# Performance work log

Measured on AMD Instinct MI355X. Metric: run time of the kernel, lower is better.

Reference implementation:

```python
import jax, jax.numpy as jnp
import numpy as np

T, F = 32768, 512


def setup_inputs() -> dict:
    key = jax.random.key(0)
    ks = jax.random.split(key, 7)
    return {
        "x": jax.random.normal(ks[0], (T, F), dtype=jnp.float32),
        # per-feature LSTM(1,1) params, PyTorch gate order [i, f, g, o]
        "w_ih": 0.5 * jax.random.normal(ks[1], (F, 4), dtype=jnp.float32),
        "w_hh": 0.5 * jax.random.normal(ks[2], (F, 4), dtype=jnp.float32),
        "b_ih": 0.5 * jax.random.normal(ks[3], (F, 4), dtype=jnp.float32),
        "b_hh": 0.5 * jax.random.normal(ks[4], (F, 4), dtype=jnp.float32),
        # torch.rand for h0, torch.randn for c0 (as in the original forward)
        "h0": jax.random.uniform(ks[5], (F,), dtype=jnp.float32),
        "c0": jax.random.normal(ks[6], (F,), dtype=jnp.float32),
    }


def reference(x, w_ih, w_hh, b_ih, b_hh, h0, c0):
    # Fused: all F independent scalar LSTM cells stepped together over time.
    b = b_ih + b_hh  # [F, 4]

    def step(carry, x_t):
        h, c = carry  # [F], [F]
        gates = x_t[:, None] * w_ih + h[:, None] * w_hh + b  # [F, 4]
        i = jax.nn.sigmoid(gates[:, 0])
        f = jax.nn.sigmoid(gates[:, 1])
        g = jnp.tanh(gates[:, 2])
        o = jax.nn.sigmoid(gates[:, 3])
        c = f * c + i * g
        h = o * jnp.tanh(c)
        return (h, c), 2.0 * h  # forward emits 2 * out

    _, ys = jax.lax.scan(step, (h0, c0), x)
    return ys  # [T, F]
```

## Files before the change

kernel.cpp:

```cpp
#include <hip/hip_runtime.h>


#define T_STEPS 32768
#define F_FEAT  512
#define CHUNK_L 64
#define WARM    96
#define DEPTH   (WARM + CHUNK_L)
#define UNROLL  8

typedef float v2f __attribute__((ext_vector_type(2)));

__device__ __forceinline__ v2f pk_fma(v2f a, v2f b, v2f c) {
    return __builtin_elementwise_fma(a, b, c);
}
__device__ __forceinline__ v2f exp2v(v2f a) {
    v2f r; r.x = __builtin_amdgcn_exp2f(a.x); r.y = __builtin_amdgcn_exp2f(a.y); return r;
}
__device__ __forceinline__ v2f rcpv(v2f a) {
    v2f r; r.x = __builtin_amdgcn_rcpf(a.x); r.y = __builtin_amdgcn_rcpf(a.y); return r;
}

__global__ __launch_bounds__(64, 2) void lstm_kernel(
    const float*  __restrict__ x,
    const float4* __restrict__ w_ih,
    const float4* __restrict__ w_hh,
    const float4* __restrict__ b_ih,
    const float4* __restrict__ b_hh,
    const float*  __restrict__ h0,
    const float*  __restrict__ c0,
    float*        __restrict__ out)
{
    const int cb = blockIdx.x;
    const int f  = blockIdx.y * 64 + threadIdx.x;

    const float LOG2E = 1.4426950408889634f;
    const float S_SIG = -LOG2E;
    const float S_C   = 2.0f * LOG2E;

    const float4 wi = w_ih[f];
    const float4 wh = w_hh[f];
    const float4 bi = b_ih[f];
    const float4 bh = b_hh[f];

    const v2f W1i = S_SIG * wi.x, W1f = S_SIG * wi.y, W1g = S_C * wi.z, W1o = S_SIG * wi.w;
    const v2f W2i = 0.5f * S_SIG * wh.x, W2f = 0.5f * S_SIG * wh.y,
              W2g = 0.5f * S_C   * wh.z, W2o = 0.5f * S_SIG * wh.w;
    const v2f Bi  = S_SIG * (bi.x + bh.x);
    const v2f Bf  = S_SIG * (bi.y + bh.y);
    const v2f Bg  = S_C   * (bi.z + bh.z);
    const v2f Bo  = S_SIG * (bi.w + bh.w);

    const v2f ONE  = 1.0f;
    const v2f SCv  = S_C;
    const v2f mSCv = -S_C;
    const v2f M4   = -4.0f;
    const v2f TWO  = 2.0f;

    const int t_emitA = (2 * cb) * CHUNK_L;
    const int baseA   = t_emitA - WARM;

    v2f H2 = 0.0f, C2 = 0.0f;
    const float H0v = 2.0f * h0[f];
    const float C0v = S_C * c0[f];

    const float* xp = x + f;
    float*       op = out + f;

    float curA[UNROLL], nxtA[UNROLL], curB[UNROLL], nxtB[UNROLL];
#pragma unroll
    for (int j = 0; j < UNROLL; ++j) {
        int tA = baseA + j;           if (tA < 0) tA = 0;
        int tB = baseA + CHUNK_L + j; if (tB < 0) tB = 0;
        curA[j] = xp[tA * F_FEAT];
        curB[j] = xp[tB * F_FEAT];
        nxtA[j] = 0.0f; nxtB[j] = 0.0f;
    }

    for (int s0 = 0; s0 < DEPTH; s0 += UNROLL) {
        const int sn = s0 + UNROLL;
        if (sn < DEPTH) {
#pragma unroll
            for (int j = 0; j < UNROLL; ++j) {
                int tA = baseA + sn + j;           if (tA < 0) tA = 0;
                int tB = baseA + CHUNK_L + sn + j; if (tB < 0) tB = 0;
                nxtA[j] = xp[tA * F_FEAT];
                nxtB[j] = xp[tB * F_FEAT];
            }
        }
        if (cb == 0) {
            if (s0 == WARM - CHUNK_L) { H2.y = H0v; C2.y = C0v; }
            if (s0 == WARM)           { H2.x = H0v; C2.x = C0v; }
        }
        const bool emit = (s0 >= WARM);
#pragma unroll
        for (int j = 0; j < UNROLL; ++j) {
            const v2f xv = { curA[j], curB[j] };
            v2f gi = pk_fma(xv, W1i, Bi); gi = pk_fma(H2, W2i, gi);
            v2f gf = pk_fma(xv, W1f, Bf); gf = pk_fma(H2, W2f, gf);
            v2f gg = pk_fma(xv, W1g, Bg); gg = pk_fma(H2, W2g, gg);
            v2f go = pk_fma(xv, W1o, Bo); go = pk_fma(H2, W2o, go);
            const v2f ui = exp2v(gi);
            const v2f uf = exp2v(gf);
            const v2f ug = exp2v(gg);
            const v2f uo = exp2v(go);
            const v2f ai = ui + ONE;
            const v2f af = uf + ONE;
            const v2f ag = ug + ONE;
            const v2f ao = uo + ONE;
            const v2f am = pk_fma(ug, SCv, mSCv);
            const v2f P  = ai * ag;
            const v2f D  = P * af;
            const v2f D3 = D * ao;
            const v2f t2 = am * af;
            const v2f N  = pk_fma(C2, P, t2);
            const v2f R  = rcpv(D3);
            const v2f N2 = N * ao;
            C2 = N2 * R;
            const v2f ro = D * R;
            const v2f e  = exp2v(C2);
            const v2f ae = e + ONE;
            const v2f cc = rcpv(ae);
            const v2f TH = pk_fma(cc, M4, TWO);
            H2 = ro * TH;
            if (emit) {
                const int tw = t_emitA + (s0 - WARM) + j;
                op[tw * F_FEAT]             = H2.x;
                op[(tw + CHUNK_L) * F_FEAT] = H2.y;
            }
        }
#pragma unroll
        for (int j = 0; j < UNROLL; ++j) { curA[j] = nxtA[j]; curB[j] = nxtB[j]; }
    }
}

extern "C" void kernel_launch(void* const* d_in, const int* in_sizes, int n_in,
                              void* d_out, int out_size, void* d_ws, size_t ws_size,
                              hipStream_t stream) {
    const float*  x    = (const float*)d_in[0];
    const float4* w_ih = (const float4*)d_in[1];
    const float4* w_hh = (const float4*)d_in[2];
    const float4* b_ih = (const float4*)d_in[3];
    const float4* b_hh = (const float4*)d_in[4];
    const float*  h0   = (const float*)d_in[5];
    const float*  c0   = (const float*)d_in[6];
    float* out = (float*)d_out;

    lstm_kernel<<<dim3(T_STEPS / (2 * CHUNK_L), F_FEAT / 64), dim3(64), 0, stream>>>(
        x, w_ih, w_hh, b_ih, b_hh, h0, c0, out);
}
```

Baseline: 155.7 us.

## Fold output gate into recurrent weights to shorten serial dependency chain

Splits h into tanh(c) times the output-gate reciprocal and multiplies that reciprocal into the per-step recurrent weights, so the output gate's rcp runs off the critical path and the single combined rcp is replaced by two shorter independent ones. The h-dependent chain loses a multiply, at the cost of an extra rcp and four extra multiplies per step. It also specializes x-loading for blocks with nonnegative base index to drop the clamping. Numerics change slightly because of the separate reciprocals.

```diff
diff --git a/kernel.cpp b/kernel.cpp
--- a/kernel.cpp
+++ b/kernel.cpp
@@ -43,8 +43,8 @@
     const float4 bh = b_hh[f];
 
     const v2f W1i = S_SIG * wi.x, W1f = S_SIG * wi.y, W1g = S_C * wi.z, W1o = S_SIG * wi.w;
-    const v2f W2i = 0.5f * S_SIG * wh.x, W2f = 0.5f * S_SIG * wh.y,
-              W2g = 0.5f * S_C   * wh.z, W2o = 0.5f * S_SIG * wh.w;
+    const float W2i_s = 0.5f * S_SIG * wh.x, W2f_s = 0.5f * S_SIG * wh.y,
+                W2g_s = 0.5f * S_C   * wh.z, W2o_s = 0.5f * S_SIG * wh.w;
     const v2f Bi  = S_SIG * (bi.x + bh.x);
     const v2f Bf  = S_SIG * (bi.y + bh.y);
     const v2f Bg  = S_C   * (bi.z + bh.z);
@@ -59,7 +59,8 @@
     const int t_emitA = (2 * cb) * CHUNK_L;
     const int baseA   = t_emitA - WARM;
 
-    v2f H2 = 0.0f, C2 = 0.0f;
+    v2f th2 = 0.0f, C2 = 0.0f;
+    v2f W2roI = W2i_s, W2roF = W2f_s, W2roG = W2g_s, W2roO = W2o_s;
     const float H0v = 2.0f * h0[f];
     const float C0v = S_C * c0[f];
 
@@ -67,38 +68,61 @@
     float*       op = out + f;
 
     float curA[UNROLL], nxtA[UNROLL], curB[UNROLL], nxtB[UNROLL];
+    if (baseA >= 0) {
 #pragma unroll
-    for (int j = 0; j < UNROLL; ++j) {
-        int tA = baseA + j;           if (tA < 0) tA = 0;
-        int tB = baseA + CHUNK_L + j; if (tB < 0) tB = 0;
-        curA[j] = xp[tA * F_FEAT];
-        curB[j] = xp[tB * F_FEAT];
-        nxtA[j] = 0.0f; nxtB[j] = 0.0f;
+        for (int j = 0; j < UNROLL; ++j) {
+            curA[j] = xp[(baseA + j) * F_FEAT];
+            curB[j] = xp[(baseA + CHUNK_L + j) * F_FEAT];
+            nxtA[j] = 0.0f; nxtB[j] = 0.0f;
+        }
+    } else {
+#pragma unroll
+        for (int j = 0; j < UNROLL; ++j) {
+            int tA = baseA + j;           if (tA < 0) tA = 0;
+            int tB = baseA + CHUNK_L + j; if (tB < 0) tB = 0;
+            curA[j] = xp[tA * F_FEAT];
+            curB[j] = xp[tB * F_FEAT];
+            nxtA[j] = 0.0f; nxtB[j] = 0.0f;
+        }
     }
 
     for (int s0 = 0; s0 < DEPTH; s0 += UNROLL) {
         const int sn = s0 + UNROLL;
         if (sn < DEPTH) {
+            if (baseA >= 0) {
 #pragma unroll
-            for (int j = 0; j < UNROLL; ++j) {
-                int tA = baseA + sn + j;           if (tA < 0) tA = 0;
-                int tB = baseA + CHUNK_L + sn + j; if (tB < 0) tB = 0;
-                nxtA[j] = xp[tA * F_FEAT];
-                nxtB[j] = xp[tB * F_FEAT];
+                for (int j = 0; j < UNROLL; ++j) {
+                    nxtA[j] = xp[(baseA + sn + j) * F_FEAT];
+                    nxtB[j] = xp[(baseA + CHUNK_L + sn + j) * F_FEAT];
+                }
+            } else {
+#pragma unroll
+                for (int j = 0; j < UNROLL; ++j) {
+                    int tA = baseA + sn + j;           if (tA < 0) tA = 0;
+                    int tB = baseA + CHUNK_L + sn + j; if (tB < 0) tB = 0;
+                    nxtA[j] = xp[tA * F_FEAT];
+                    nxtB[j] = xp[tB * F_FEAT];
+                }
             }
         }
         if (cb == 0) {
-            if (s0 == WARM - CHUNK_L) { H2.y = H0v; C2.y = C0v; }
-            if (s0 == WARM)           { H2.x = H0v; C2.x = C0v; }
+            if (s0 == WARM - CHUNK_L) {
+                th2.y = H0v; C2.y = C0v;
+                W2roI.y = W2i_s; W2roF.y = W2f_s; W2roG.y = W2g_s; W2roO.y = W2o_s;
+            }
+            if (s0 == WARM) {
+                th2.x = H0v; C2.x = C0v;
+                W2roI.x = W2i_s; W2roF.x = W2f_s; W2roG.x = W2g_s; W2roO.x = W2o_s;
+            }
         }
         const bool emit = (s0 >= WARM);
 #pragma unroll
         for (int j = 0; j < UNROLL; ++j) {
             const v2f xv = { curA[j], curB[j] };
-            v2f gi = pk_fma(xv, W1i, Bi); gi = pk_fma(H2, W2i, gi);
-            v2f gf = pk_fma(xv, W1f, Bf); gf = pk_fma(H2, W2f, gf);
-            v2f gg = pk_fma(xv, W1g, Bg); gg = pk_fma(H2, W2g, gg);
-            v2f go = pk_fma(xv, W1o, Bo); go = pk_fma(H2, W2o, go);
+            v2f gi = pk_fma(xv, W1i, Bi); gi = pk_fma(th2, W2roI, gi);
+            v2f gf = pk_fma(xv, W1f, Bf); gf = pk_fma(th2, W2roF, gf);
+            v2f gg = pk_fma(xv, W1g, Bg); gg = pk_fma(th2, W2roG, gg);
+            v2f go = pk_fma(xv, W1o, Bo); go = pk_fma(th2, W2roO, go);
             const v2f ui = exp2v(gi);
             const v2f uf = exp2v(gf);
             const v2f ug = exp2v(gg);
@@ -107,25 +131,25 @@
             const v2f af = uf + ONE;
             const v2f ag = ug + ONE;
             const v2f ao = uo + ONE;
+            const v2f ro = rcpv(ao);
             const v2f am = pk_fma(ug, SCv, mSCv);
             const v2f P  = ai * ag;
-            const v2f D  = P * af;
-            const v2f D3 = D * ao;
+            const v2f Q  = P * af;
             const v2f t2 = am * af;
+            const v2f R3 = rcpv(Q);
             const v2f N  = pk_fma(C2, P, t2);
-            const v2f R  = rcpv(D3);
-            const v2f N2 = N * ao;
-            C2 = N2 * R;
-            const v2f ro = D * R;
+            C2 = N * R3;
             const v2f e  = exp2v(C2);
             const v2f ae = e + ONE;
             const v2f cc = rcpv(ae);
-            const v2f TH = pk_fma(cc, M4, TWO);
-            H2 = ro * TH;
+            th2 = pk_fma(cc, M4, TWO);
+            W2roI = W2i_s * ro; W2roF = W2f_s * ro;
+            W2roG = W2g_s * ro; W2roO = W2o_s * ro;
             if (emit) {
+                const v2f H = th2 * ro;
                 const int tw = t_emitA + (s0 - WARM) + j;
-                op[tw * F_FEAT]             = H2.x;
-                op[(tw + CHUNK_L) * F_FEAT] = H2.y;
+                op[tw * F_FEAT]             = H.x;
+                op[(tw + CHUNK_L) * F_FEAT] = H.y;
             }
         }
 #pragma unroll
```

Result: faster. 147.4 us (-5.3%).

## Ping-pong x prefetch buffers, drop clamps off-edge, shorten recurrence dependency chain

Applied to the files above, without the earlier changes.

Replaces the cur/next buffer copy with an even/odd ping-pong scheme, so each half-iteration's loads are issued while the other half computes and the register copies go away. Blocks whose window does not start before t=0 skip the clamp logic on addresses. The cell math is also reordered: the output-gate reciprocal is computed on its own and the cell update divides by a three-factor product instead of a four-factor one. This shortens the serial chain through C2 at the cost of one extra reciprocal per step. The emit condition is evaluated per 16-step pair, and since WARM is a multiple of 16 it stays correct.

```diff
diff --git a/kernel.cpp b/kernel.cpp
--- a/kernel.cpp
+++ b/kernel.cpp
@@ -66,25 +66,72 @@
     const float* xp = x + f;
     float*       op = out + f;
 
-    float curA[UNROLL], nxtA[UNROLL], curB[UNROLL], nxtB[UNROLL];
+    float eA[UNROLL], eB[UNROLL], oA[UNROLL], oB[UNROLL];
+    if (baseA >= 0) {
 #pragma unroll
-    for (int j = 0; j < UNROLL; ++j) {
-        int tA = baseA + j;           if (tA < 0) tA = 0;
-        int tB = baseA + CHUNK_L + j; if (tB < 0) tB = 0;
-        curA[j] = xp[tA * F_FEAT];
-        curB[j] = xp[tB * F_FEAT];
-        nxtA[j] = 0.0f; nxtB[j] = 0.0f;
+        for (int j = 0; j < UNROLL; ++j) {
+            eA[j] = xp[(baseA + j) * F_FEAT];
+            eB[j] = xp[(baseA + CHUNK_L + j) * F_FEAT];
+        }
+    } else {
+#pragma unroll
+        for (int j = 0; j < UNROLL; ++j) {
+            int tA = baseA + j;           if (tA < 0) tA = 0;
+            int tB = baseA + CHUNK_L + j; if (tB < 0) tB = 0;
+            eA[j] = xp[tA * F_FEAT];
+            eB[j] = xp[tB * F_FEAT];
+        }
     }
 
-    for (int s0 = 0; s0 < DEPTH; s0 += UNROLL) {
-        const int sn = s0 + UNROLL;
-        if (sn < DEPTH) {
+#define STEP(xa, xb, tw_expr)                                            \
+    {                                                                    \
+        const v2f xv = { (xa), (xb) };                                   \
+        v2f gi = pk_fma(xv, W1i, Bi); gi = pk_fma(H2, W2i, gi);          \
+        v2f gf = pk_fma(xv, W1f, Bf); gf = pk_fma(H2, W2f, gf);          \
+        v2f gg = pk_fma(xv, W1g, Bg); gg = pk_fma(H2, W2g, gg);          \
+        v2f go = pk_fma(xv, W1o, Bo); go = pk_fma(H2, W2o, go);          \
+        const v2f ui = exp2v(gi);                                        \
+        const v2f uf = exp2v(gf);                                        \
+        const v2f ug = exp2v(gg);                                        \
+        const v2f uo = exp2v(go);                                        \
+        const v2f ai = ui + ONE;                                         \
+        const v2f af = uf + ONE;                                         \
+        const v2f ag = ug + ONE;                                         \
+        const v2f ao = uo + ONE;                                         \
+        const v2f ro = rcpv(ao);                            \
+        const v2f am = pk_fma(ug, SCv, mSCv);            \
+        const v2f P  = ai * ag;                                          \
+        const v2f Q  = P * af;                                           \
+        const v2f t2 = am * af;                                          \
+        const v2f R3 = rcpv(Q);                                          \
+        const v2f N  = pk_fma(C2, P, t2);                                \
+        C2 = N * R3;                                  \
+        const v2f e  = exp2v(C2);                                        \
+        const v2f ae = e + ONE;                                          \
+        const v2f cc = rcpv(ae);                                         \
+        const v2f th2 = pk_fma(cc, M4, TWO);              \
+        H2 = th2 * ro;                                         \
+        if (emit) {                                                      \
+            const int tw = (tw_expr);                                    \
+            op[tw * F_FEAT]             = H2.x;                          \
+            op[(tw + CHUNK_L) * F_FEAT] = H2.y;                          \
+        }                                                                \
+    }
+
+    for (int s0 = 0; s0 < DEPTH; s0 += 2 * UNROLL) {
+        if (baseA >= 0) {
 #pragma unroll
             for (int j = 0; j < UNROLL; ++j) {
-                int tA = baseA + sn + j;           if (tA < 0) tA = 0;
-                int tB = baseA + CHUNK_L + sn + j; if (tB < 0) tB = 0;
-                nxtA[j] = xp[tA * F_FEAT];
-                nxtB[j] = xp[tB * F_FEAT];
+                oA[j] = xp[(baseA + s0 + UNROLL + j) * F_FEAT];
+                oB[j] = xp[(baseA + CHUNK_L + s0 + UNROLL + j) * F_FEAT];
+            }
+        } else {
+#pragma unroll
+            for (int j = 0; j < UNROLL; ++j) {
+                int tA = baseA + s0 + UNROLL + j;           if (tA < 0) tA = 0;
+                int tB = baseA + CHUNK_L + s0 + UNROLL + j; if (tB < 0) tB = 0;
+                oA[j] = xp[tA * F_FEAT];
+                oB[j] = xp[tB * F_FEAT];
             }
         }
         if (cb == 0) {
@@ -93,44 +140,31 @@
         }
         const bool emit = (s0 >= WARM);
 #pragma unroll
-        for (int j = 0; j < UNROLL; ++j) {
-            const v2f xv = { curA[j], curB[j] };
-            v2f gi = pk_fma(xv, W1i, Bi); gi = pk_fma(H2, W2i, gi);
-            v2f gf = pk_fma(xv, W1f, Bf); gf = pk_fma(H2, W2f, gf);
-            v2f gg = pk_fma(xv, W1g, Bg); gg = pk_fma(H2, W2g, gg);
-            v2f go = pk_fma(xv, W1o, Bo); go = pk_fma(H2, W2o, go);
-            const v2f ui = exp2v(gi);
-            const v2f uf = exp2v(gf);
-            const v2f ug = exp2v(gg);
-            const v2f uo = exp2v(go);
-            const v2f ai = ui + ONE;
-            const v2f af = uf + ONE;
-            const v2f ag = ug + ONE;
-            const v2f ao = uo + ONE;
-            const v2f am = pk_fma(ug, SCv, mSCv);
-            const v2f P  = ai * ag;
-            const v2f D  = P * af;
-            const v2f D3 = D * ao;
-            const v2f t2 = am * af;
-            const v2f N  = pk_fma(C2, P, t2);
-            const v2f R  = rcpv(D3);
-            const v2f N2 = N * ao;
-            C2 = N2 * R;
-            const v2f ro = D * R;
-            const v2f e  = exp2v(C2);
-            const v2f ae = e + ONE;
-            const v2f cc = rcpv(ae);
-            const v2f TH = pk_fma(cc, M4, TWO);
-            H2 = ro * TH;
-            if (emit) {
-                const int tw = t_emitA + (s0 - WARM) + j;
-                op[tw * F_FEAT]             = H2.x;
-                op[(tw + CHUNK_L) * F_FEAT] = H2.y;
+        for (int j = 0; j < UNROLL; ++j)
+            STEP(eA[j], eB[j], t_emitA + (s0 - WARM) + j);
+        const int sn = s0 + 2 * UNROLL;
+        if (sn < DEPTH) {
+            if (baseA >= 0) {
+#pragma unroll
+                for (int j = 0; j < UNROLL; ++j) {
+                    eA[j] = xp[(baseA + sn + j) * F_FEAT];
+                    eB[j] = xp[(baseA + CHUNK_L + sn + j) * F_FEAT];
+                }
+            } else {
+#pragma unroll
+                for (int j = 0; j < UNROLL; ++j) {
+                    int tA = baseA + sn + j;           if (tA < 0) tA = 0;
+                    int tB = baseA + CHUNK_L + sn + j; if (tB < 0) tB = 0;
+                    eA[j] = xp[tA * F_FEAT];
+                    eB[j] = xp[tB * F_FEAT];
+                }
             }
         }
 #pragma unroll
-        for (int j = 0; j < UNROLL; ++j) { curA[j] = nxtA[j]; curB[j] = nxtB[j]; }
+        for (int j = 0; j < UNROLL; ++j)
+            STEP(oA[j], oB[j], t_emitA + (s0 - WARM) + UNROLL + j);
     }
+#undef STEP
 }
 
 extern "C" void kernel_launch(void* const* d_in, const int* in_sizes, int n_in,
```

New measurement: 150.5 us. -3.3%, faster.

## Shorten warmup, drop clamping on interior chunks, split reciprocal off critical path

Applied to the files above, without the earlier changes.

Cuts the warm-up recurrence length from 96 to 88 steps, so each block runs fewer sequential steps at the cost of a slightly less converged state when the chunk starts emitting. Adds a branch that skips the index clamping when the chunk start is non-negative. Restructures the gate algebra so the output-gate sigmoid uses its own reciprocal, independent of the cell-state path, which shortens the serial dependency chain on C but adds one extra rcp per step. Reducing the warm-up relies on the recurrence forgetting its initial state, which carries an accuracy risk.

```diff
diff --git a/kernel.cpp b/kernel.cpp
--- a/kernel.cpp
+++ b/kernel.cpp
@@ -4,7 +4,7 @@
 #define T_STEPS 32768
 #define F_FEAT  512
 #define CHUNK_L 64
-#define WARM    96
+#define WARM    88
 #define DEPTH   (WARM + CHUNK_L)
 #define UNROLL  8
 
@@ -67,24 +67,41 @@
     float*       op = out + f;
 
     float curA[UNROLL], nxtA[UNROLL], curB[UNROLL], nxtB[UNROLL];
+    if (baseA >= 0) {
 #pragma unroll
-    for (int j = 0; j < UNROLL; ++j) {
-        int tA = baseA + j;           if (tA < 0) tA = 0;
-        int tB = baseA + CHUNK_L + j; if (tB < 0) tB = 0;
-        curA[j] = xp[tA * F_FEAT];
-        curB[j] = xp[tB * F_FEAT];
-        nxtA[j] = 0.0f; nxtB[j] = 0.0f;
+        for (int j = 0; j < UNROLL; ++j) {
+            curA[j] = xp[(baseA + j) * F_FEAT];
+            curB[j] = xp[(baseA + CHUNK_L + j) * F_FEAT];
+            nxtA[j] = 0.0f; nxtB[j] = 0.0f;
+        }
+    } else {
+#pragma unroll
+        for (int j = 0; j < UNROLL; ++j) {
+            int tA = baseA + j;           if (tA < 0) tA = 0;
+            int tB = baseA + CHUNK_L + j; if (tB < 0) tB = 0;
+            curA[j] = xp[tA * F_FEAT];
+            curB[j] = xp[tB * F_FEAT];
+            nxtA[j] = 0.0f; nxtB[j] = 0.0f;
+        }
     }
 
     for (int s0 = 0; s0 < DEPTH; s0 += UNROLL) {
         const int sn = s0 + UNROLL;
         if (sn < DEPTH) {
+            if (baseA >= 0) {
 #pragma unroll
-            for (int j = 0; j < UNROLL; ++j) {
-                int tA = baseA + sn + j;           if (tA < 0) tA = 0;
-                int tB = baseA + CHUNK_L + sn + j; if (tB < 0) tB = 0;
-                nxtA[j] = xp[tA * F_FEAT];
-                nxtB[j] = xp[tB * F_FEAT];
+                for (int j = 0; j < UNROLL; ++j) {
+                    nxtA[j] = xp[(baseA + sn + j) * F_FEAT];
+                    nxtB[j] = xp[(baseA + CHUNK_L + sn + j) * F_FEAT];
+                }
+            } else {
+#pragma unroll
+                for (int j = 0; j < UNROLL; ++j) {
+                    int tA = baseA + sn + j;           if (tA < 0) tA = 0;
+                    int tB = baseA + CHUNK_L + sn + j; if (tB < 0) tB = 0;
+                    nxtA[j] = xp[tA * F_FEAT];
+                    nxtB[j] = xp[tB * F_FEAT];
+                }
             }
         }
         if (cb == 0) {
@@ -107,21 +124,19 @@
             const v2f af = uf + ONE;
             const v2f ag = ug + ONE;
             const v2f ao = uo + ONE;
+            const v2f ro = rcpv(ao);
             const v2f am = pk_fma(ug, SCv, mSCv);
             const v2f P  = ai * ag;
-            const v2f D  = P * af;
-            const v2f D3 = D * ao;
+            const v2f Q  = P * af;
             const v2f t2 = am * af;
+            const v2f R3 = rcpv(Q);
             const v2f N  = pk_fma(C2, P, t2);
-            const v2f R  = rcpv(D3);
-            const v2f N2 = N * ao;
-            C2 = N2 * R;
-            const v2f ro = D * R;
+            C2 = N * R3;
             const v2f e  = exp2v(C2);
             const v2f ae = e + ONE;
             const v2f cc = rcpv(ae);
-            const v2f TH = pk_fma(cc, M4, TWO);
-            H2 = ro * TH;
+            const v2f th2 = pk_fma(cc, M4, TWO);
+            H2 = th2 * ro;
             if (emit) {
                 const int tw = t_emitA + (s0 - WARM) + j;
                 op[tw * F_FEAT]             = H2.x;
```

Result: faster. 143.9 us (-7.6%).
